# Optimization experiments

Hardware: AMD Instinct MI355X
Metric: run time of the kernel (lower is better)

The kernel has to match this reference:

```python
import jax, jax.numpy as jnp
import numpy as np

N = 65536      # nodes
E = 196608     # edges
G = 2048       # graphs
F_IN = 9
D = 128        # output_dim
H1 = 10        # heads layer 1
NEG_SLOPE = 0.2


def _gat_layer(x, src, dst, W, a_src, a_dst, bias, heads, out_c, concat):
    """PyG GATConv (add_self_loops already applied to src/dst)."""
    n = x.shape[0]
    h = (x @ W).reshape(n, heads, out_c)                     # [N,H,C]
    alpha_s = (h * a_src).sum(-1)                            # [N,H]
    alpha_d = (h * a_dst).sum(-1)                            # [N,H]
    e = jax.nn.leaky_relu(alpha_s[src] + alpha_d[dst], NEG_SLOPE)  # [E,H]
    # segment softmax over destination node
    m = jax.ops.segment_max(e, dst, num_segments=n)          # [N,H]
    ex = jnp.exp(e - m[dst])
    denom = jax.ops.segment_sum(ex, dst, num_segments=n)
    alpha = ex / (denom[dst] + 1e-16)                        # [E,H]
    out = jax.ops.segment_sum(h[src] * alpha[:, :, None], dst, num_segments=n)  # [N,H,C]
    out = out.reshape(n, heads * out_c) if concat else out.mean(1)
    return out + bias


def setup_inputs() -> dict:
    key = jax.random.key(0)
    ks = jax.random.split(key, 16)
    x = jax.random.normal(ks[0], (N, F_IN), dtype=jnp.float32)
    edge_index = jax.random.randint(ks[1], (2, E), 0, N, dtype=jnp.int64)
    edge_attr = jax.random.normal(ks[2], (E,), dtype=jnp.float32)  # unused by forward
    batch = jnp.sort(jax.random.randint(ks[3], (N,), 0, G, dtype=jnp.int64))
    s = 0.1
    params = {
        "W1": jax.random.normal(ks[4], (F_IN, H1 * D), dtype=jnp.float32) * s,
        "a_src1": jax.random.normal(ks[5], (H1, D), dtype=jnp.float32) * s,
        "a_dst1": jax.random.normal(ks[6], (H1, D), dtype=jnp.float32) * s,
        "b1": jnp.zeros((H1 * D,), dtype=jnp.float32),
        "W2": jax.random.normal(ks[7], (H1 * D, D), dtype=jnp.float32) * s,
        "a_src2": jax.random.normal(ks[8], (1, D), dtype=jnp.float32) * s,
        "a_dst2": jax.random.normal(ks[9], (1, D), dtype=jnp.float32) * s,
        "b2": jnp.zeros((D,), dtype=jnp.float32),
        "Wfc": jax.random.normal(ks[10], (D, D), dtype=jnp.float32) * s,
        "bfc": jnp.zeros((D,), dtype=jnp.float32),
    }
    return {"x": x, "edge_index": edge_index, "edge_attr": edge_attr, "batch": batch, **params}


def reference(x, edge_index, edge_attr, batch,
              W1, a_src1, a_dst1, b1, W2, a_src2, a_dst2, b2, Wfc, bfc):
    # GATConv default add_self_loops=True
    loops = jnp.arange(N, dtype=edge_index.dtype)
    src = jnp.concatenate([edge_index[0], loops])
    dst = jnp.concatenate([edge_index[1], loops])

    x1 = _gat_layer(x, src, dst, W1, a_src1, a_dst1, b1, H1, D, concat=True)
    x1 = jax.nn.elu(x1)                       # dropout = identity (eval)
    x1 = _gat_layer(x1, src, dst, W2, a_src2, a_dst2, b2, 1, D, concat=False)
    x1 = jax.nn.elu(x1)

    pooled = jax.ops.segment_max(x1, batch, num_segments=G)   # [G,D]
    pooled = jnp.where(jnp.isfinite(pooled), pooled, 0.0)      # guard empty graphs
    out = jax.nn.relu(pooled @ Wfc + bfc)
    return out
```

## Files before the change

### kernel.cpp

```cpp
#include <hip/hip_runtime.h>
#include <hip/hip_bf16.h>
#include <math.h>

#define NN 65536
#define NE 196608
#define ET (NE + NN)
#define NG 2048
#define FIN 9
#define DD 128
#define H1 10
#define KK (H1 * DD)
#define LRS 0.2f
#define XSB 36

typedef __attribute__((ext_vector_type(8))) short short8v;
typedef __attribute__((ext_vector_type(4))) float f32x4;

__device__ __forceinline__ float lrelu(float v) { return v >= 0.f ? v : LRS * v; }
__device__ __forceinline__ float eluf(float v)  { return v > 0.f ? v : expm1f(v); }

__device__ __forceinline__ unsigned short f2bf(float f) {
    unsigned int u = __float_as_uint(f);
    u += 0x7FFFu + ((u >> 16) & 1u);
    return (unsigned short)(u >> 16);
}
__device__ __forceinline__ float bf2f(unsigned short s) {
    return __uint_as_float((unsigned int)s << 16);
}

__global__ __launch_bounds__(256) void setup_kernel(
        const float* __restrict__ W1, const float* __restrict__ W2,
        const float* __restrict__ a_src1, const float* __restrict__ a_dst1,
        const float* __restrict__ x, const int* __restrict__ batch,
        const int* __restrict__ ei,
        unsigned short* __restrict__ W2p, unsigned short* __restrict__ W1pT,
        float* __restrict__ as1, float* __restrict__ ad1,
        int* __restrict__ deg, int* __restrict__ gptr) {
    __shared__ float ws_s[FIN * H1], wd_s[FIN * H1];
    const int b = blockIdx.x;
    const int t = threadIdx.x;
    if (b < 640) {
        int idx = b * 256 + t;
        int r  = idx & 7;
        int l  = (idx >> 3) & 63;
        int nt = (idx >> 9) & 7;
        int kt = idx >> 12;
        int k = kt * 32 + ((l >> 4) << 3) + r;
        int n = nt * 16 + (l & 15);
        W2p[idx] = f2bf(W2[(size_t)k * DD + n]);
    } else if (b < 896) {
        if (t < FIN * H1) {
            int f = t / H1, h = t - f * H1;
            float s = 0.f, d = 0.f;
            for (int c = 0; c < DD; ++c) {
                float w = W1[f * KK + h * DD + c];
                s = fmaf(w, a_src1[h * DD + c], s);
                d = fmaf(w, a_dst1[h * DD + c], d);
            }
            ws_s[t] = s;
            wd_s[t] = d;
        }
        __syncthreads();
        int n = (b - 640) * 256 + t;
        float xv[FIN];
#pragma unroll
        for (int f = 0; f < FIN; ++f) xv[f] = x[(size_t)n * FIN + f];
#pragma unroll
        for (int h = 0; h < H1; ++h) {
            float s = 0.f, d = 0.f;
#pragma unroll
            for (int f = 0; f < FIN; ++f) {
                s = fmaf(xv[f], ws_s[f * H1 + h], s);
                d = fmaf(xv[f], wd_s[f * H1 + h], d);
            }
            as1[n * H1 + h] = s;
            ad1[n * H1 + h] = d;
        }
    } else if (b < 1152) {
        int n = (b - 896) * 256 + t;
        int bn = batch[n];
        int bp = (n == 0) ? -1 : batch[n - 1];
        for (int g = bp + 1; g <= bn; ++g) gptr[g] = n;
        if (n == NN - 1) {
            for (int g = bn + 1; g <= NG; ++g) gptr[g] = NN;
        }
    } else if (b < 1312) {
        int idx = (b - 1152) * 256 + t;
        int r  = idx & 7;
        int l  = (idx >> 3) & 63;
        int mt = (idx >> 9) & 7;
        int h  = idx >> 12;
        int f  = ((l >> 4) << 3) + r;
        int c  = mt * 16 + (l & 15);
        W1pT[idx] = (f < FIN) ? f2bf(W1[(size_t)f * KK + h * DD + c]) : (unsigned short)0;
    } else {
        int e = (b - 1312) * 256 + t;
        if (e < ET) {
            int d = (e < NE) ? ei[NE + e] : e - NE;
            atomicAdd(&deg[d], 1);
        }
    }
}

__global__ __launch_bounds__(256) void scan1_kernel(const int* __restrict__ deg,
                                                    int* __restrict__ bsum) {
    __shared__ int sc[256];
    int t = threadIdx.x, b = blockIdx.x;
    sc[t] = deg[b * 256 + t];
    __syncthreads();
    for (int off = 128; off > 0; off >>= 1) {
        if (t < off) sc[t] += sc[t + off];
        __syncthreads();
    }
    if (t == 0) bsum[b] = sc[0];
}

__global__ __launch_bounds__(256) void scan23_kernel(const int* __restrict__ deg,
                                                     const int* __restrict__ bsum,
                                                     int* __restrict__ rowptr,
                                                     int* __restrict__ cursor) {
    __shared__ int sb[256], sc[256];
    int t = threadIdx.x, b = blockIdx.x;
    sb[t] = bsum[t];
    int i = b * 256 + t;
    int v = deg[i];
    sc[t] = v;
    __syncthreads();
    for (int off = 1; off < 256; off <<= 1) {
        int ub = (t >= off) ? sb[t - off] : 0;
        int uc = (t >= off) ? sc[t - off] : 0;
        __syncthreads();
        sb[t] += ub;
        sc[t] += uc;
        __syncthreads();
    }
    int base = (b == 0) ? 0 : sb[b - 1];
    int r = base + sc[t] - v;
    rowptr[i] = r;
    cursor[i] = r;
    if (b == 255 && t == 255) rowptr[NN] = sb[255];
}

__global__ void scatter_kernel(const int* __restrict__ ei, int* __restrict__ cursor,
                               int* __restrict__ elist) {
    int e = blockIdx.x * 256 + threadIdx.x;
    if (e >= ET) return;
    int s, d;
    if (e < NE) { s = ei[e]; d = ei[NE + e]; } else { s = d = e - NE; }
    int pos = atomicAdd(&cursor[d], 1);
    elist[pos] = s;
}

__global__ void agg1_kernel(const int* __restrict__ rowptr, const int* __restrict__ elist,
                            const float* __restrict__ x,
                            const float* __restrict__ as1, const float* __restrict__ ad1,
                            unsigned short* __restrict__ xaggb) {
    int idx = blockIdx.x * 256 + threadIdx.x;
    if (idx >= NN * H1) return;
    int d = idx / H1, h = idx - d * H1;
    int beg = rowptr[d], end = rowptr[d + 1];
    float adh = ad1[d * H1 + h];
    float m = -INFINITY, den = 0.f;
    float xa[FIN] = {};
    {
        int s0 = elist[beg];
        int sB = (beg + 1 < end) ? elist[beg + 1] : s0;
        float asv = as1[s0 * H1 + h];
        float xs[FIN];
#pragma unroll
        for (int f = 0; f < FIN; ++f) xs[f] = x[(size_t)s0 * FIN + f];
        for (int j = beg; j < end; ++j) {
            int sC = (j + 2 < end) ? elist[j + 2] : sB;
            float asn = 0.f, xn[FIN];
            if (j + 1 < end) {
                asn = as1[sB * H1 + h];
#pragma unroll
                for (int f = 0; f < FIN; ++f) xn[f] = x[(size_t)sB * FIN + f];
            }
            float v = lrelu(asv + adh);
            if (v > m) {
                float sc = __expf(m - v);
                den *= sc;
#pragma unroll
                for (int f = 0; f < FIN; ++f) xa[f] *= sc;
                m = v;
            }
            float ex = __expf(v - m);
            den += ex;
#pragma unroll
            for (int f = 0; f < FIN; ++f) xa[f] = fmaf(ex, xs[f], xa[f]);
            if (j + 1 < end) {
                asv = asn;
#pragma unroll
                for (int f = 0; f < FIN; ++f) xs[f] = xn[f];
            }
            sB = sC;
        }
    }
    float inv = 1.f / (den + 1e-16f);
    unsigned int w[16];
#pragma unroll
    for (int i = 0; i < 16; ++i) w[i] = 0u;
#pragma unroll
    for (int f = 0; f < FIN; ++f) {
        unsigned int bv = f2bf(xa[f] * inv);
        w[f >> 1] |= bv << ((f & 1) * 16);
    }
    uint4* dst = (uint4*)&xaggb[(size_t)idx * 32];
    dst[0] = make_uint4(w[0], w[1], w[2], w[3]);
    dst[1] = make_uint4(w[4], w[5], w[6], w[7]);
    dst[2] = make_uint4(w[8], w[9], w[10], w[11]);
    dst[3] = make_uint4(w[12], w[13], w[14], w[15]);
}

__global__ __launch_bounds__(512, 4) void h2_gemm(
        const unsigned short* __restrict__ xaggb,
        const unsigned short* __restrict__ W1pT,
        const float* __restrict__ b1,
        const unsigned short* __restrict__ W2p,
        const float* __restrict__ a_src2, const float* __restrict__ a_dst2,
        unsigned short* __restrict__ h2b, float* __restrict__ as2,
        float* __restrict__ ad2) {
    __shared__ unsigned short Xs0[128 * 64];
    __shared__ unsigned short Xs1[128 * 64];
    __shared__ unsigned short xsb[2][128 * XSB];
    __shared__ float as_s[128], ad_s[128];
    const int t = threadIdx.x;
    const int n0 = blockIdx.x * 128;
    const int lane = t & 63;
    const int wvu = __builtin_amdgcn_readfirstlane(t >> 6);
    const int rh = wvu & 1, cq = wvu >> 1;
    const int rlo = lane & 15, khi = lane >> 4;
    const int srow = t >> 2, sseg = t & 3;

    if (t < 128) { as_s[t] = 0.f; ad_s[t] = 0.f; }

    f32x4 acc[4][2];
#pragma unroll
    for (int mt = 0; mt < 4; ++mt)
#pragma unroll
        for (int ntl = 0; ntl < 2; ++ntl)
#pragma unroll
            for (int q = 0; q < 4; ++q) acc[mt][ntl][q] = 0.f;

    *(uint4*)&xsb[0][srow * XSB + sseg * 8] =
        *(const uint4*)&xaggb[((size_t)(n0 + srow) * H1 + 0) * 32 + sseg * 8];

    for (int h = 0; h < H1; ++h) {
        const int cur = h & 1;
        __syncthreads();

        short8v a1 = *(const short8v*)&W1pT[(((size_t)h * 8 + wvu) * 64 + lane) * 8];
        float4 bv4 = *(const float4*)&b1[h * DD + wvu * 16 + khi * 4];
        unsigned short* XsW = (wvu >> 2) ? Xs1 : Xs0;
        const int gw7 = (wvu * 2 + (khi >> 1)) & 7;
#pragma unroll
        for (int nh = 0; nh < 2; ++nh) {
            f32x4 acc2[4];
#pragma unroll
            for (int j = 0; j < 4; ++j) {
                int nt = nh * 4 + j;
                short8v bfrag = *(const short8v*)&xsb[cur][(nt * 16 + rlo) * XSB + khi * 8];
                f32x4 zz = {0.f, 0.f, 0.f, 0.f};
                acc2[j] = __builtin_amdgcn_mfma_f32_16x16x32_bf16(a1, bfrag, zz, 0, 0, 0);
            }
#pragma unroll
            for (int j = 0; j < 4; ++j) {
                int nt = nh * 4 + j;
                float z0 = acc2[j][0] + bv4.x;
                float z1 = acc2[j][1] + bv4.y;
                float z2 = acc2[j][2] + bv4.z;
                float z3 = acc2[j][3] + bv4.w;
                z0 = z0 > 0.f ? z0 : __expf(z0) - 1.f;
                z1 = z1 > 0.f ? z1 : __expf(z1) - 1.f;
                z2 = z2 > 0.f ? z2 : __expf(z2) - 1.f;
                z3 = z3 > 0.f ? z3 : __expf(z3) - 1.f;
                unsigned int lo = (unsigned int)f2bf(z0) | ((unsigned int)f2bf(z1) << 16);
                unsigned int hi = (unsigned int)f2bf(z2) | ((unsigned int)f2bf(z3) << 16);
                int rown = nt * 16 + rlo;
                unsigned offu = rown * 64 + (((gw7 ^ (rown & 7)) << 3) | ((khi & 1) << 2));
                *(uint2*)&XsW[offu] = make_uint2(lo, hi);
            }
        }
        __syncthreads();

        if (h + 1 < H1) {
            *(uint4*)&xsb[cur ^ 1][srow * XSB + sseg * 8] =
                *(const uint4*)&xaggb[((size_t)(n0 + srow) * H1 + (h + 1)) * 32 + sseg * 8];
        }

#pragma unroll
        for (int ks = 0; ks < 4; ++ks) {
            const int ktabs = h * 4 + ks;
            const unsigned short* XsR = (ks >> 1) ? Xs1 : Xs0;
            const int g7 = (ks & 1) * 4 + khi;
            short8v bfr[2];
#pragma unroll
            for (int ntl = 0; ntl < 2; ++ntl) {
                const int nt = cq * 2 + ntl;
                bfr[ntl] = *(const short8v*)&W2p[(((size_t)ktabs * 8 + nt) * 64 + lane) * 8];
            }
#pragma unroll
            for (int mt = 0; mt < 4; ++mt) {
                const int row2 = rh * 64 + mt * 16 + rlo;
                unsigned offu = row2 * 64 + ((g7 ^ (row2 & 7)) << 3);
                short8v af = *(const short8v*)&XsR[offu];
                acc[mt][0] = __builtin_amdgcn_mfma_f32_16x16x32_bf16(af, bfr[0], acc[mt][0], 0, 0, 0);
                acc[mt][1] = __builtin_amdgcn_mfma_f32_16x16x32_bf16(af, bfr[1], acc[mt][1], 0, 0, 0);
            }
        }
    }

    __syncthreads();
#pragma unroll
    for (int mt = 0; mt < 4; ++mt)
#pragma unroll
        for (int ntl = 0; ntl < 2; ++ntl) {
            int col = cq * 32 + ntl * 16 + rlo;
            unsigned short* Xw = (col < 64) ? Xs0 : Xs1;
            int c64 = col & 63;
#pragma unroll
            for (int q = 0; q < 4; ++q) {
                int row = rh * 64 + mt * 16 + khi * 4 + q;
                Xw[row * 64 + c64] = f2bf(acc[mt][ntl][q]);
            }
        }
    __syncthreads();
#pragma unroll
    for (int i = 0; i < 4; ++i) {
        int j = i * 512 + t;
        int row = j >> 4;
        int c8 = (j & 15) * 8;
        const unsigned short* S = (c8 < 64) ? Xs0 : Xs1;
        uint4 v = *(const uint4*)&S[row * 64 + (c8 & 63)];
        *(uint4*)&h2b[(size_t)(n0 + row) * DD + c8] = v;
    }

    float sp[16], dp[16];
#pragma unroll
    for (int mt = 0; mt < 4; ++mt)
#pragma unroll
        for (int q = 0; q < 4; ++q) {
            float a = 0.f, b = 0.f;
#pragma unroll
            for (int ntl = 0; ntl < 2; ++ntl) {
                int col = cq * 32 + ntl * 16 + rlo;
                float v = acc[mt][ntl][q];
                a = fmaf(v, a_src2[col], a);
                b = fmaf(v, a_dst2[col], b);
            }
            sp[mt * 4 + q] = a;
            dp[mt * 4 + q] = b;
        }
#pragma unroll
    for (int off = 1; off < 16; off <<= 1) {
#pragma unroll
        for (int i = 0; i < 16; ++i) {
            sp[i] += __shfl_xor(sp[i], off);
            dp[i] += __shfl_xor(dp[i], off);
        }
    }
    if (rlo == 0) {
#pragma unroll
        for (int mt = 0; mt < 4; ++mt)
#pragma unroll
            for (int q = 0; q < 4; ++q) {
                atomicAdd(&as_s[rh * 64 + mt * 16 + khi * 4 + q], sp[mt * 4 + q]);
                atomicAdd(&ad_s[rh * 64 + mt * 16 + khi * 4 + q], dp[mt * 4 + q]);
            }
    }
    __syncthreads();
    if (t < 128) {
        as2[n0 + t] = as_s[t];
        ad2[n0 + t] = ad_s[t];
    }
}

__global__ void agg2_kernel(const int* __restrict__ rowptr, const int* __restrict__ elist,
                            const unsigned short* __restrict__ h2b,
                            const float* __restrict__ as2, const float* __restrict__ ad2,
                            const float* __restrict__ b2, unsigned short* __restrict__ x2b) {
    int gid = blockIdx.x * 256 + threadIdx.x;
    int n = gid >> 5, lane = gid & 31;
    if (n >= NN) return;
    int beg = rowptr[n], end = rowptr[n + 1];
    float adn = ad2[n];
    float m = -INFINITY, den = 0.f;
    float4 acc = make_float4(0.f, 0.f, 0.f, 0.f);
    {
        int s0 = elist[beg];
        int sB = (beg + 1 < end) ? elist[beg + 1] : s0;
        float asv = as2[s0];
        ushort4 hv = *(const ushort4*)&h2b[(size_t)s0 * DD + lane * 4];
        for (int j = beg; j < end; ++j) {
            int sC = (j + 2 < end) ? elist[j + 2] : sB;
            float asn = 0.f;
            ushort4 hn = make_ushort4(0, 0, 0, 0);
            if (j + 1 < end) {
                asn = as2[sB];
                hn = *(const ushort4*)&h2b[(size_t)sB * DD + lane * 4];
            }
            float v = lrelu(asv + adn);
            if (v > m) {
                float sc = __expf(m - v);
                den *= sc;
                acc.x *= sc; acc.y *= sc; acc.z *= sc; acc.w *= sc;
                m = v;
            }
            float ex = __expf(v - m);
            den += ex;
            acc.x = fmaf(ex, bf2f(hv.x), acc.x);
            acc.y = fmaf(ex, bf2f(hv.y), acc.y);
            acc.z = fmaf(ex, bf2f(hv.z), acc.z);
            acc.w = fmaf(ex, bf2f(hv.w), acc.w);
            if (j + 1 < end) { asv = asn; hv = hn; }
            sB = sC;
        }
    }
    float inv = 1.f / (den + 1e-16f);
    float4 bv = *(const float4*)&b2[lane * 4];
    ushort4 o;
    o.x = f2bf(eluf(acc.x * inv + bv.x));
    o.y = f2bf(eluf(acc.y * inv + bv.y));
    o.z = f2bf(eluf(acc.z * inv + bv.z));
    o.w = f2bf(eluf(acc.w * inv + bv.w));
    *(ushort4*)&x2b[(size_t)n * DD + lane * 4] = o;
}

__global__ __launch_bounds__(128) void pool_final_kernel(const int* __restrict__ gptr,
                                                         const unsigned short* __restrict__ x2b,
                                                         const float* __restrict__ Wfc,
                                                         const float* __restrict__ bfc,
                                                         float* __restrict__ out) {
    __shared__ float pl[DD];
    int g = blockIdx.x;
    int c = threadIdx.x;
    int beg = gptr[g], end = gptr[g + 1];
    float v = -INFINITY;
    for (int n = beg; n < end; ++n)
        v = fmaxf(v, bf2f(x2b[(size_t)n * DD + c]));
    if (beg == end) v = 0.f;
    pl[c] = v;
    __syncthreads();
    float acc = bfc[c];
#pragma unroll 8
    for (int k = 0; k < DD; ++k)
        acc = fmaf(pl[k], Wfc[k * DD + c], acc);
    out[(size_t)g * DD + c] = acc > 0.f ? acc : 0.f;
}

extern "C" void kernel_launch(void* const* d_in, const int* in_sizes, int n_in,
                              void* d_out, int out_size, void* d_ws, size_t ws_size,
                              hipStream_t stream) {
    const float* x      = (const float*)d_in[0];
    const int*   ei     = (const int*)d_in[1];
    const int*   batch  = (const int*)d_in[3];
    const float* W1     = (const float*)d_in[4];
    const float* a_src1 = (const float*)d_in[5];
    const float* a_dst1 = (const float*)d_in[6];
    const float* b1     = (const float*)d_in[7];
    const float* W2     = (const float*)d_in[8];
    const float* a_src2 = (const float*)d_in[9];
    const float* a_dst2 = (const float*)d_in[10];
    const float* b2     = (const float*)d_in[11];
    const float* Wfc    = (const float*)d_in[12];
    const float* bfc    = (const float*)d_in[13];
    float* out = (float*)d_out;

    float* wsf    = (float*)d_ws;
    float* as1    = wsf;
    float* ad1    = as1 + (size_t)NN * H1;
    float* as2    = ad1 + (size_t)NN * H1;
    float* ad2    = as2 + NN;
    int*   deg    = (int*)(ad2 + NN);
    int*   rowptr = deg + NN;
    int*   cursor = rowptr + NN + 1;
    int*   elist  = cursor + NN;
    int*   gptr   = elist + ET;
    int*   bsum   = gptr + NG + 1;
    size_t off = (size_t)((char*)(bsum + 256) - (char*)d_ws);
    off = (off + 15) & ~(size_t)15;
    unsigned short* W2p   = (unsigned short*)((char*)d_ws + off);
    unsigned short* W1pT  = W2p + (size_t)KK * DD;
    unsigned short* xaggb = W1pT + 40960;
    unsigned short* h2b   = xaggb + (size_t)NN * H1 * 32;
    unsigned short* x2b   = h2b + (size_t)NN * DD;

    hipMemsetAsync(deg, 0, (size_t)NN * sizeof(int), stream);
    setup_kernel     <<<1312 + (ET + 255) / 256, 256, 0, stream>>>(
                        W1, W2, a_src1, a_dst1, x, batch, ei,
                        W2p, W1pT, as1, ad1, deg, gptr);
    scan1_kernel     <<<256, 256, 0, stream>>>(deg, bsum);
    scan23_kernel    <<<256, 256, 0, stream>>>(deg, bsum, rowptr, cursor);
    scatter_kernel   <<<(ET + 255) / 256, 256, 0, stream>>>(ei, cursor, elist);
    agg1_kernel      <<<(NN * H1 + 255) / 256, 256, 0, stream>>>(rowptr, elist, x, as1, ad1, xaggb);
    h2_gemm          <<<NN / 128, 512, 0, stream>>>(xaggb, W1pT, b1, W2p, a_src2, a_dst2,
                                                    h2b, as2, ad2);
    agg2_kernel      <<<(NN * 32) / 256, 256, 0, stream>>>(rowptr, elist, h2b, as2, ad2, b2, x2b);
    pool_final_kernel<<<NG, 128, 0, stream>>>(gptr, x2b, Wfc, bfc, out);
}
```

Before: 155.7 us.

## Halve h2_gemm LDS staging buffer by processing each head in two halves

The per-head ELU tile buffer is cut from two 128x64 bf16 arrays to one. Each head is now handled in two 64-column halves, with an extra barrier pair per half, and the epilogue reuses the xsb buffer as its second staging area. The smaller LDS footprint is meant to let more blocks stay resident per CU. In exchange the number of __syncthreads per head doubles and each layer-1 phase has half the MFMA work to hide latency behind.

```diff
diff --git a/kernel.cpp b/kernel.cpp
--- a/kernel.cpp
+++ b/kernel.cpp
@@ -221,8 +221,7 @@
         const float* __restrict__ a_src2, const float* __restrict__ a_dst2,
         unsigned short* __restrict__ h2b, float* __restrict__ as2,
         float* __restrict__ ad2) {
-    __shared__ unsigned short Xs0[128 * 64];
-    __shared__ unsigned short Xs1[128 * 64];
+    __shared__ unsigned short Xs[128 * 64];
     __shared__ unsigned short xsb[2][128 * XSB];
     __shared__ float as_s[128], ad_s[128];
     const int t = threadIdx.x;
@@ -230,6 +229,7 @@
     const int lane = t & 63;
     const int wvu = __builtin_amdgcn_readfirstlane(t >> 6);
     const int rh = wvu & 1, cq = wvu >> 1;
+    const int ct = wvu & 3, nh2 = wvu >> 2;
     const int rlo = lane & 15, khi = lane >> 4;
     const int srow = t >> 2, sseg = t & 3;
 
@@ -248,25 +248,25 @@
 
     for (int h = 0; h < H1; ++h) {
         const int cur = h & 1;
-        __syncthreads();
-
-        short8v a1 = *(const short8v*)&W1pT[(((size_t)h * 8 + wvu) * 64 + lane) * 8];
-        float4 bv4 = *(const float4*)&b1[h * DD + wvu * 16 + khi * 4];
-        unsigned short* XsW = (wvu >> 2) ? Xs1 : Xs0;
-        const int gw7 = (wvu * 2 + (khi >> 1)) & 7;
-#pragma unroll
-        for (int nh = 0; nh < 2; ++nh) {
+#pragma unroll
+        for (int half = 0; half < 2; ++half) {
+            __syncthreads();
+
+            short8v a1 = *(const short8v*)
+                &W1pT[(((size_t)h * 8 + half * 4 + ct) * 64 + lane) * 8];
+            float4 bv4 = *(const float4*)&b1[h * DD + half * 64 + ct * 16 + khi * 4];
+            const int gw7 = ct * 2 + (khi >> 1);
             f32x4 acc2[4];
 #pragma unroll
             for (int j = 0; j < 4; ++j) {
-                int nt = nh * 4 + j;
+                int nt = nh2 * 4 + j;
                 short8v bfrag = *(const short8v*)&xsb[cur][(nt * 16 + rlo) * XSB + khi * 8];
                 f32x4 zz = {0.f, 0.f, 0.f, 0.f};
                 acc2[j] = __builtin_amdgcn_mfma_f32_16x16x32_bf16(a1, bfrag, zz, 0, 0, 0);
             }
 #pragma unroll
             for (int j = 0; j < 4; ++j) {
-                int nt = nh * 4 + j;
+                int nt = nh2 * 4 + j;
                 float z0 = acc2[j][0] + bv4.x;
                 float z1 = acc2[j][1] + bv4.y;
                 float z2 = acc2[j][2] + bv4.z;
@@ -279,45 +279,45 @@
                 unsigned int hi = (unsigned int)f2bf(z2) | ((unsigned int)f2bf(z3) << 16);
                 int rown = nt * 16 + rlo;
                 unsigned offu = rown * 64 + (((gw7 ^ (rown & 7)) << 3) | ((khi & 1) << 2));
-                *(uint2*)&XsW[offu] = make_uint2(lo, hi);
-            }
-        }
-        __syncthreads();
-
-        if (h + 1 < H1) {
-            *(uint4*)&xsb[cur ^ 1][srow * XSB + sseg * 8] =
-                *(const uint4*)&xaggb[((size_t)(n0 + srow) * H1 + (h + 1)) * 32 + sseg * 8];
-        }
-
-#pragma unroll
-        for (int ks = 0; ks < 4; ++ks) {
-            const int ktabs = h * 4 + ks;
-            const unsigned short* XsR = (ks >> 1) ? Xs1 : Xs0;
-            const int g7 = (ks & 1) * 4 + khi;
-            short8v bfr[2];
-#pragma unroll
-            for (int ntl = 0; ntl < 2; ++ntl) {
-                const int nt = cq * 2 + ntl;
-                bfr[ntl] = *(const short8v*)&W2p[(((size_t)ktabs * 8 + nt) * 64 + lane) * 8];
-            }
-#pragma unroll
-            for (int mt = 0; mt < 4; ++mt) {
-                const int row2 = rh * 64 + mt * 16 + rlo;
-                unsigned offu = row2 * 64 + ((g7 ^ (row2 & 7)) << 3);
-                short8v af = *(const short8v*)&XsR[offu];
-                acc[mt][0] = __builtin_amdgcn_mfma_f32_16x16x32_bf16(af, bfr[0], acc[mt][0], 0, 0, 0);
-                acc[mt][1] = __builtin_amdgcn_mfma_f32_16x16x32_bf16(af, bfr[1], acc[mt][1], 0, 0, 0);
+                *(uint2*)&Xs[offu] = make_uint2(lo, hi);
+            }
+            __syncthreads();
+
+            if (half == 0 && h + 1 < H1) {
+                *(uint4*)&xsb[cur ^ 1][srow * XSB + sseg * 8] =
+                    *(const uint4*)&xaggb[((size_t)(n0 + srow) * H1 + (h + 1)) * 32 + sseg * 8];
+            }
+
+#pragma unroll
+            for (int ks2 = 0; ks2 < 2; ++ks2) {
+                const int ktabs = h * 4 + half * 2 + ks2;
+                const int g7 = ks2 * 4 + khi;
+                short8v bfr[2];
+#pragma unroll
+                for (int ntl = 0; ntl < 2; ++ntl) {
+                    const int nt = cq * 2 + ntl;
+                    bfr[ntl] = *(const short8v*)&W2p[(((size_t)ktabs * 8 + nt) * 64 + lane) * 8];
+                }
+#pragma unroll
+                for (int mt = 0; mt < 4; ++mt) {
+                    const int row2 = rh * 64 + mt * 16 + rlo;
+                    unsigned offu = row2 * 64 + ((g7 ^ (row2 & 7)) << 3);
+                    short8v af = *(const short8v*)&Xs[offu];
+                    acc[mt][0] = __builtin_amdgcn_mfma_f32_16x16x32_bf16(af, bfr[0], acc[mt][0], 0, 0, 0);
+                    acc[mt][1] = __builtin_amdgcn_mfma_f32_16x16x32_bf16(af, bfr[1], acc[mt][1], 0, 0, 0);
+                }
             }
         }
     }
 
     __syncthreads();
+    unsigned short* xsbf = &xsb[0][0];
 #pragma unroll
     for (int mt = 0; mt < 4; ++mt)
 #pragma unroll
         for (int ntl = 0; ntl < 2; ++ntl) {
             int col = cq * 32 + ntl * 16 + rlo;
-            unsigned short* Xw = (col < 64) ? Xs0 : Xs1;
+            unsigned short* Xw = (col < 64) ? Xs : xsbf;
             int c64 = col & 63;
 #pragma unroll
             for (int q = 0; q < 4; ++q) {
@@ -331,7 +331,7 @@
         int j = i * 512 + t;
         int row = j >> 4;
         int c8 = (j & 15) * 8;
-        const unsigned short* S = (c8 < 64) ? Xs0 : Xs1;
+        const unsigned short* S = (c8 < 64) ? Xs : xsbf;
         uint4 v = *(const uint4*)&S[row * 64 + (c8 & 63)];
         *(uint4*)&h2b[(size_t)(n0 + row) * DD + c8] = v;
     }
```

After: 159.6 us. +2.5%, slower.
